# Performance work log

Measured on AMD Instinct MI355X. Metric: run time of the kernel, lower is better.

## Reference

```python
import jax, jax.numpy as jnp
import numpy as np

T, B, IN = 216, 16384, 8
H1, H2 = 16, 64


def _lstm_scan(xs, h0, c0, Wih, Whh, bih, bhh):
    # xs: [T, B, D_in]; returns all hidden states [T, B, H]
    def step(carry, x_t):
        h, c = carry
        g = x_t @ Wih.T + bih + h @ Whh.T + bhh  # [B, 4H]
        i, f, gg, o = jnp.split(g, 4, axis=-1)
        c = jax.nn.sigmoid(f) * c + jax.nn.sigmoid(i) * jnp.tanh(gg)
        h = jax.nn.sigmoid(o) * jnp.tanh(c)
        return (h, c), h
    (_, _), hs = jax.lax.scan(step, (h0, c0), xs)
    return hs


def setup_inputs() -> dict:
    key = jax.random.key(0)
    ks = jax.random.split(key, 24)
    def rn(k, shape, std):
        return jax.random.normal(k, shape, dtype=jnp.float32) * std
    # PyTorch LSTMCell/Linear default init: U(-1/sqrt(H), 1/sqrt(H)) -> use uniform
    def un(k, shape, bound):
        return jax.random.uniform(k, shape, dtype=jnp.float32, minval=-bound, maxval=bound)
    b1 = 1.0 / np.sqrt(H1)
    b2 = 1.0 / np.sqrt(H2)
    inp = {
        'x': jax.random.normal(ks[0], (T, B, IN), dtype=jnp.float32),
        # initial states: kaiming_normal_ with fan_in = last dim -> std = sqrt(2/fan_in)
        'h0f': rn(ks[1], (B, H1), np.sqrt(2.0 / H1)),
        'c0f': rn(ks[2], (B, H1), np.sqrt(2.0 / H1)),
        'h0b': rn(ks[3], (B, H1), np.sqrt(2.0 / H1)),
        'c0b': rn(ks[4], (B, H1), np.sqrt(2.0 / H1)),
        'h0m': rn(ks[5], (B, H2), np.sqrt(2.0 / H2)),
        'c0m': rn(ks[6], (B, H2), np.sqrt(2.0 / H2)),
        'Wih_f': un(ks[7], (4 * H1, IN), b1), 'Whh_f': un(ks[8], (4 * H1, H1), b1),
        'bih_f': un(ks[9], (4 * H1,), b1), 'bhh_f': un(ks[10], (4 * H1,), b1),
        'Wih_b': un(ks[11], (4 * H1, IN), b1), 'Whh_b': un(ks[12], (4 * H1, H1), b1),
        'bih_b': un(ks[13], (4 * H1,), b1), 'bhh_b': un(ks[14], (4 * H1,), b1),
        'Wih_m': un(ks[15], (4 * H2, 2 * H1), b2), 'Whh_m': un(ks[16], (4 * H2, H2), b2),
        'bih_m': un(ks[17], (4 * H2,), b2), 'bhh_m': un(ks[18], (4 * H2,), b2),
        'Wd': un(ks[19], (1, H2), b2), 'bd': un(ks[20], (1,), b2),
    }
    return inp


def reference(x, h0f, c0f, h0b, c0b, h0m, c0m,
              Wih_f, Whh_f, bih_f, bhh_f,
              Wih_b, Whh_b, bih_b, bhh_b,
              Wih_m, Whh_m, bih_m, bhh_m,
              Wd, bd):
    # forward direction LSTM over time
    hs_f = _lstm_scan(x, h0f, c0f, Wih_f, Whh_f, bih_f, bhh_f)          # [T,B,16]
    # backward direction: run on reversed sequence, then reverse outputs
    hs_b = _lstm_scan(x[::-1], h0b, c0b, Wih_b, Whh_b, bih_b, bhh_b)[::-1]  # [T,B,16]
    mid_in = jnp.concatenate([hs_f, hs_b], axis=-1)                     # [T,B,32]
    hs_m = _lstm_scan(mid_in, h0m, c0m, Wih_m, Whh_m, bih_m, bhh_m)     # [T,B,64]
    # dropout is identity in inference reference; dense 64->1 per step
    out = jnp.einsum('tbh,oh->tbo', hs_m, Wd) + bd                      # [T,B,1]
    return out[:, :, 0].T                                                # [B,T]
```

## Files before the change

kernel.cpp:

```cpp
#include <hip/hip_runtime.h>

#define TT 216
#define BB 16384
#define LOG2E 1.44269504088896340736f

typedef _Float16 h16;
typedef _Float16 half8 __attribute__((ext_vector_type(8)));
typedef float f32x4 __attribute__((ext_vector_type(4)));

__device__ __forceinline__ float rcp_f(float v) { return __builtin_amdgcn_rcpf(v); }
__device__ __forceinline__ float ex2(float v)   { return __builtin_amdgcn_exp2f(v); }

__device__ __forceinline__ float lstm_up(float pi, float pf, float pg, float po, float& cs)
{
    float ei = ex2(pi), ef = ex2(pf), eg = ex2(pg), eo = ex2(po);
    float Ei = 1.f + ei, Ef = 1.f + ef, Eg = 1.f + eg, Eo = 1.f + eo;
    float EiEg = Ei * Eg;
    float G = fmaf(2.f * LOG2E, Eg, -4.f * LOG2E);
    float N = fmaf(cs, EiEg, Ef * G);
    cs = N * rcp_f(Ef * EiEg);
    float pc = fminf(cs, 60.f);
    float Ec = 1.f + ex2(pc);
    return (Ec - 2.f) * rcp_f(Eo * Ec);
}

__global__ void prep_kernel(
    const float* __restrict__ Wih_f, const float* __restrict__ Whh_f,
    const float* __restrict__ bih_f, const float* __restrict__ bhh_f,
    const float* __restrict__ Wih_b, const float* __restrict__ Whh_b,
    const float* __restrict__ bih_b, const float* __restrict__ bhh_b,
    const float* __restrict__ Wih_m, const float* __restrict__ Whh_m,
    const float* __restrict__ bih_m, const float* __restrict__ bhh_m,
    h16* __restrict__ W1f, h16* __restrict__ W1b, h16* __restrict__ W2)
{
    int gtid = blockIdx.x * blockDim.x + threadIdx.x;
    int gs = gridDim.x * blockDim.x;
    for (int idx = gtid; idx < 64 * 32; idx += gs) {
        int n = idx >> 5, k = idx & 31;
        float a = ((n >> 4) == 2) ? 2.f * LOG2E : -LOG2E;
        float vf = 0.f, vb = 0.f;
        if (k < 8)        { vf = Wih_f[n * 8 + k];       vb = Wih_b[n * 8 + k]; }
        else if (k < 24)  { vf = Whh_f[n * 16 + k - 8];  vb = Whh_b[n * 16 + k - 8]; }
        else if (k == 24) { vf = bih_f[n] + bhh_f[n];    vb = bih_b[n] + bhh_b[n]; }
        W1f[idx] = (h16)(vf * a);
        W1b[idx] = (h16)(vb * a);
    }
    for (int idx = gtid; idx < 256 * 128; idx += gs) {
        int n = idx >> 7, k = idx & 127;
        float a = ((n >> 6) == 2) ? 2.f * LOG2E : -LOG2E;
        float v = 0.f;
        if (k < 32)       v = Wih_m[n * 32 + k];
        else if (k < 96)  v = Whh_m[n * 64 + k - 32];
        else if (k == 96) v = bih_m[n] + bhh_m[n];
        W2[idx] = (h16)(v * a);
    }
}

__global__ __launch_bounds__(256, 2) void small_lstm_kernel(
    const float* __restrict__ x,
    const float* __restrict__ h0f, const float* __restrict__ c0f,
    const float* __restrict__ h0b, const float* __restrict__ c0b,
    const h16* __restrict__ W1f, const h16* __restrict__ W1b,
    h16* __restrict__ hsf, h16* __restrict__ hsb)
{
    __shared__ __attribute__((aligned(16))) h16 hbuf[4][16][24];

    const int tid = threadIdx.x;
    const int wv = tid >> 6, lane = tid & 63;
    const int b = lane & 15, q = lane >> 4;

    const int wgid = blockIdx.x * 4 + wv;
    const int dir  = wgid & 1;
    const int base = (wgid >> 1) * 16;

    const float* h0 = dir ? h0b : h0f;
    const float* c0 = dir ? c0b : c0f;
    const h16* W1   = dir ? W1b : W1f;
    h16* hs = dir ? hsb : hsf;

    half8 bf0 = *(const half8*)(W1 + (0 * 16 + b) * 32 + q * 8);
    half8 bf1 = *(const half8*)(W1 + (1 * 16 + b) * 32 + q * 8);
    half8 bf2 = *(const half8*)(W1 + (2 * 16 + b) * 32 + q * 8);
    half8 bf3 = *(const half8*)(W1 + (3 * 16 + b) * 32 + q * 8);

    float cs0 = c0[(size_t)(base + q * 4 + 0) * 16 + b] * (2.f * LOG2E);
    float cs1 = c0[(size_t)(base + q * 4 + 1) * 16 + b] * (2.f * LOG2E);
    float cs2 = c0[(size_t)(base + q * 4 + 2) * 16 + b] * (2.f * LOG2E);
    float cs3 = c0[(size_t)(base + q * 4 + 3) * 16 + b] * (2.f * LOG2E);

    const int t0 = dir ? (TT - 1) : 0;
    const int t1 = dir ? (TT - 2) : 1;

    half8 af;
    if (q == 0) {
        const float* xp = x + ((size_t)t0 * BB + base + b) * 8;
        f32x4 u0 = *(const f32x4*)xp, u1 = *(const f32x4*)(xp + 4);
        af[0] = (h16)u0[0]; af[1] = (h16)u0[1]; af[2] = (h16)u0[2]; af[3] = (h16)u0[3];
        af[4] = (h16)u1[0]; af[5] = (h16)u1[1]; af[6] = (h16)u1[2]; af[7] = (h16)u1[3];
    } else if (q == 3) {
        af[0] = (h16)1.f;
        af[1] = (h16)0.f; af[2] = (h16)0.f; af[3] = (h16)0.f;
        af[4] = (h16)0.f; af[5] = (h16)0.f; af[6] = (h16)0.f; af[7] = (h16)0.f;
    } else {
        const float* hp = h0 + (size_t)(base + b) * 16 + (q - 1) * 8;
        f32x4 u0 = *(const f32x4*)hp, u1 = *(const f32x4*)(hp + 4);
        af[0] = (h16)u0[0]; af[1] = (h16)u0[1]; af[2] = (h16)u0[2]; af[3] = (h16)u0[3];
        af[4] = (h16)u1[0]; af[5] = (h16)u1[1]; af[6] = (h16)u1[2]; af[7] = (h16)u1[3];
    }

    f32x4 xf0 = {0.f, 0.f, 0.f, 0.f}, xf1 = {0.f, 0.f, 0.f, 0.f};
    if (q == 0) {
        const float* xp = x + ((size_t)t1 * BB + base + b) * 8;
        xf0 = *(const f32x4*)xp;
        xf1 = *(const f32x4*)(xp + 4);
    }

    for (int s = 0; s < TT; ++s) {
        const int t = dir ? (TT - 1 - s) : s;

        f32x4 z0 = {0.f, 0.f, 0.f, 0.f}, z1 = z0, z2 = z0, z3 = z0;
        z0 = __builtin_amdgcn_mfma_f32_16x16x32_f16(af, bf0, z0, 0, 0, 0);
        z1 = __builtin_amdgcn_mfma_f32_16x16x32_f16(af, bf1, z1, 0, 0, 0);
        z2 = __builtin_amdgcn_mfma_f32_16x16x32_f16(af, bf2, z2, 0, 0, 0);
        z3 = __builtin_amdgcn_mfma_f32_16x16x32_f16(af, bf3, z3, 0, 0, 0);

        half8 xh;
        xh[0] = (h16)xf0[0]; xh[1] = (h16)xf0[1]; xh[2] = (h16)xf0[2]; xh[3] = (h16)xf0[3];
        xh[4] = (h16)xf1[0]; xh[5] = (h16)xf1[1]; xh[6] = (h16)xf1[2]; xh[7] = (h16)xf1[3];
        {
            int sl = (s + 2 < TT) ? (s + 2) : (TT - 1);
            int tl = dir ? (TT - 1 - sl) : sl;
            if (q == 0) {
                const float* xp = x + ((size_t)tl * BB + base + b) * 8;
                xf0 = *(const f32x4*)xp;
                xf1 = *(const f32x4*)(xp + 4);
            }
        }

        float hh0 = lstm_up(z0[0], z1[0], z2[0], z3[0], cs0);
        float hh1 = lstm_up(z0[1], z1[1], z2[1], z3[1], cs1);
        float hh2 = lstm_up(z0[2], z1[2], z2[2], z3[2], cs2);
        float hh3 = lstm_up(z0[3], z1[3], z2[3], z3[3], cs3);

        hbuf[wv][q * 4 + 0][b] = (h16)hh0;
        hbuf[wv][q * 4 + 1][b] = (h16)hh1;
        hbuf[wv][q * 4 + 2][b] = (h16)hh2;
        hbuf[wv][q * 4 + 3][b] = (h16)hh3;
        asm volatile("s_waitcnt lgkmcnt(0)" ::: "memory");
        half8 hv = *(const half8*)&hbuf[wv][b][(q == 2) ? 8 : 0];

        if (q == 1 || q == 2)
            *(half8*)(hs + ((size_t)t * BB + base + b) * 16 + (q - 1) * 8) = hv;

        if (q == 0)      af = xh;
        else if (q != 3) af = hv;
    }
}

__global__ __launch_bounds__(256, 4) void mid_lstm_kernel(
    const h16* __restrict__ hsf, const h16* __restrict__ hsb,
    const float* __restrict__ h0m, const float* __restrict__ c0m,
    const h16* __restrict__ W2,
    const float* __restrict__ Wd, const float* __restrict__ bdp,
    float* __restrict__ out)
{
    __shared__ __attribute__((aligned(16))) h16 Xs[2][16][104];
    __shared__ float outbuf[16][55];

    const int tid = threadIdx.x;
    const int base = blockIdx.x * 16;
    const int wv = tid >> 6, lane = tid & 63, col = lane & 15, q = lane >> 4;

    half8 bfr[4][3];
    float bp[4];
#pragma unroll
    for (int p = 0; p < 4; ++p) {
        int n = p * 64 + wv * 16 + col;
#pragma unroll
        for (int kt = 0; kt < 3; ++kt)
            bfr[p][kt] = *(const half8*)(W2 + (size_t)n * 128 + kt * 32 + q * 8);
        bp[p] = (float)W2[(size_t)n * 128 + 96];
    }
    half8 dfr[2];
#pragma unroll
    for (int kt = 0; kt < 2; ++kt)
#pragma unroll
        for (int j = 0; j < 8; ++j)
            dfr[kt][j] = (col == 0) ? (h16)Wd[kt * 32 + q * 8 + j] : (h16)0.f;
    const float bdv = bdp[0];

    float cs[4];
#pragma unroll
    for (int r = 0; r < 4; ++r)
        cs[r] = c0m[(size_t)(base + q * 4 + r) * 64 + wv * 16 + col] * (2.f * LOG2E);

    const h16* hsrc = (wv == 1) ? hsb : hsf;
    const int srow = lane >> 1, su8 = (lane & 1) * 8;
    if (wv < 2 && lane < 32) {
        uint4 v = *(const uint4*)(hsrc + ((size_t)0 * BB + base + srow) * 16 + su8);
        *(uint4*)&Xs[0][srow][wv * 16 + su8] = v;
    }
    {
        int row = tid >> 4, u4 = (tid & 15) * 4;
        float4 v = *(const float4*)(h0m + (size_t)(base + row) * 64 + u4);
        h16* d = &Xs[0][row][32 + u4];
        d[0] = (h16)v.x; d[1] = (h16)v.y; d[2] = (h16)v.z; d[3] = (h16)v.w;
    }
    uint4 ra, rb;
    if (wv < 2 && lane < 32) {
        ra = *(const uint4*)(hsrc + ((size_t)1 * BB + base + srow) * 16 + su8);
        rb = *(const uint4*)(hsrc + ((size_t)2 * BB + base + srow) * 16 + su8);
    }
    __syncthreads();

    for (int t = 0; t < TT; ++t) {
        const int cur = t & 1, nxt = cur ^ 1;
        if (wv < 2 && lane < 32) {
            if (t < TT - 1)
                *(uint4*)&Xs[nxt][srow][wv * 16 + su8] = ra;
            ra = rb;
            int tl = (t + 3 < TT) ? (t + 3) : (TT - 1);
            rb = *(const uint4*)(hsrc + ((size_t)tl * BB + base + srow) * 16 + su8);
        }
        half8 af[3];
#pragma unroll
        for (int kt = 0; kt < 3; ++kt)
            af[kt] = *(const half8*)&Xs[cur][col][kt * 32 + q * 8];
        if (wv == 3 && t > 0) {
            f32x4 z = {0.f, 0.f, 0.f, 0.f};
            z = __builtin_amdgcn_mfma_f32_16x16x32_f16(af[1], dfr[0], z, 0, 0, 0);
            z = __builtin_amdgcn_mfma_f32_16x16x32_f16(af[2], dfr[1], z, 0, 0, 0);
            if (col == 0) {
                int tc = (t - 1) % 54;
#pragma unroll
                for (int r = 0; r < 4; ++r)
                    outbuf[q * 4 + r][tc] = z[r] + bdv;
            }
        }
        f32x4 acc[4];
#pragma unroll
        for (int p = 0; p < 4; ++p) {
            f32x4 z = {bp[p], bp[p], bp[p], bp[p]};
            z = __builtin_amdgcn_mfma_f32_16x16x32_f16(af[0], bfr[p][0], z, 0, 0, 0);
            z = __builtin_amdgcn_mfma_f32_16x16x32_f16(af[1], bfr[p][1], z, 0, 0, 0);
            z = __builtin_amdgcn_mfma_f32_16x16x32_f16(af[2], bfr[p][2], z, 0, 0, 0);
            acc[p] = z;
        }
#pragma unroll
        for (int r = 0; r < 4; ++r) {
            float h = lstm_up(acc[0][r], acc[1][r], acc[2][r], acc[3][r], cs[r]);
            Xs[nxt][q * 4 + r][32 + wv * 16 + col] = (h16)h;
        }
        if (t > 0 && (t % 54) == 0) {
            __syncthreads();
            int off = t - 54;
            for (int idx = tid; idx < 16 * 54; idx += 256) {
                int row = idx / 54, cc = idx - row * 54;
                out[(size_t)(base + row) * TT + off + cc] = outbuf[row][cc];
            }
        }
        __syncthreads();
    }
    if (wv == 3) {
        half8 a1 = *(const half8*)&Xs[0][col][32 + q * 8];
        half8 a2 = *(const half8*)&Xs[0][col][64 + q * 8];
        f32x4 z = {0.f, 0.f, 0.f, 0.f};
        z = __builtin_amdgcn_mfma_f32_16x16x32_f16(a1, dfr[0], z, 0, 0, 0);
        z = __builtin_amdgcn_mfma_f32_16x16x32_f16(a2, dfr[1], z, 0, 0, 0);
        if (col == 0)
#pragma unroll
            for (int r = 0; r < 4; ++r)
                outbuf[q * 4 + r][53] = z[r] + bdv;
    }
    __syncthreads();
    for (int idx = tid; idx < 16 * 54; idx += 256) {
        int row = idx / 54, cc = idx - row * 54;
        out[(size_t)(base + row) * TT + 162 + cc] = outbuf[row][cc];
    }
}

extern "C" void kernel_launch(void* const* d_in, const int* in_sizes, int n_in,
                              void* d_out, int out_size, void* d_ws, size_t ws_size,
                              hipStream_t stream)
{
    const float* x     = (const float*)d_in[0];
    const float* h0f   = (const float*)d_in[1];
    const float* c0f   = (const float*)d_in[2];
    const float* h0b   = (const float*)d_in[3];
    const float* c0b   = (const float*)d_in[4];
    const float* h0m   = (const float*)d_in[5];
    const float* c0m   = (const float*)d_in[6];
    const float* Wih_f = (const float*)d_in[7];
    const float* Whh_f = (const float*)d_in[8];
    const float* bih_f = (const float*)d_in[9];
    const float* bhh_f = (const float*)d_in[10];
    const float* Wih_b = (const float*)d_in[11];
    const float* Whh_b = (const float*)d_in[12];
    const float* bih_b = (const float*)d_in[13];
    const float* bhh_b = (const float*)d_in[14];
    const float* Wih_m = (const float*)d_in[15];
    const float* Whh_m = (const float*)d_in[16];
    const float* bih_m = (const float*)d_in[17];
    const float* bhh_m = (const float*)d_in[18];
    const float* Wd    = (const float*)d_in[19];
    const float* bd    = (const float*)d_in[20];

    char* ws = (char*)d_ws;
    h16* W1f = (h16*)(ws + 0);
    h16* W1b = (h16*)(ws + 4096);
    h16* W2  = (h16*)(ws + 8192);
    h16* hsf = (h16*)(ws + 73728);
    h16* hsb = (h16*)(ws + 73728 + (size_t)TT * BB * 16 * 2);

    prep_kernel<<<64, 256, 0, stream>>>(Wih_f, Whh_f, bih_f, bhh_f,
                                        Wih_b, Whh_b, bih_b, bhh_b,
                                        Wih_m, Whh_m, bih_m, bhh_m,
                                        W1f, W1b, W2);
    small_lstm_kernel<<<512, 256, 0, stream>>>(x, h0f, c0f, h0b, c0b,
                                               W1f, W1b, hsf, hsb);
    mid_lstm_kernel<<<1024, 256, 0, stream>>>(hsf, hsb, h0m, c0m, W2,
                                              Wd, bd, (float*)d_out);
}
```

Before: 669.9 us.

## Unroll bidirectional LSTM steps by four with deeper x prefetch and batched stores

The first-layer kernel now processes four timesteps per outer iteration. It keeps a four-slot register ring of prefetched x inputs, so loads are issued four steps ahead instead of two. Hidden-state stores to global memory are grouped at the end of each four-step block. The mid-LSTM kernel also raises wave priority around its MFMA block. The aim is to hide global load and store latency on the serial recurrence, at the cost of more registers and a TT divisible by 4.

```diff
diff --git a/kernel.cpp b/kernel.cpp
--- a/kernel.cpp
+++ b/kernel.cpp
@@ -89,7 +89,6 @@
     float cs3 = c0[(size_t)(base + q * 4 + 3) * 16 + b] * (2.f * LOG2E);
 
     const int t0 = dir ? (TT - 1) : 0;
-    const int t1 = dir ? (TT - 2) : 1;
 
     half8 af;
     if (q == 0) {
@@ -108,52 +107,67 @@
         af[4] = (h16)u1[0]; af[5] = (h16)u1[1]; af[6] = (h16)u1[2]; af[7] = (h16)u1[3];
     }
 
-    f32x4 xf0 = {0.f, 0.f, 0.f, 0.f}, xf1 = {0.f, 0.f, 0.f, 0.f};
+    f32x4 xr[4][2];
     if (q == 0) {
-        const float* xp = x + ((size_t)t1 * BB + base + b) * 8;
-        xf0 = *(const f32x4*)xp;
-        xf1 = *(const f32x4*)(xp + 4);
-    }
-
-    for (int s = 0; s < TT; ++s) {
-        const int t = dir ? (TT - 1 - s) : s;
-
-        f32x4 z0 = {0.f, 0.f, 0.f, 0.f}, z1 = z0, z2 = z0, z3 = z0;
-        z0 = __builtin_amdgcn_mfma_f32_16x16x32_f16(af, bf0, z0, 0, 0, 0);
-        z1 = __builtin_amdgcn_mfma_f32_16x16x32_f16(af, bf1, z1, 0, 0, 0);
-        z2 = __builtin_amdgcn_mfma_f32_16x16x32_f16(af, bf2, z2, 0, 0, 0);
-        z3 = __builtin_amdgcn_mfma_f32_16x16x32_f16(af, bf3, z3, 0, 0, 0);
-
-        half8 xh;
-        xh[0] = (h16)xf0[0]; xh[1] = (h16)xf0[1]; xh[2] = (h16)xf0[2]; xh[3] = (h16)xf0[3];
-        xh[4] = (h16)xf1[0]; xh[5] = (h16)xf1[1]; xh[6] = (h16)xf1[2]; xh[7] = (h16)xf1[3];
-        {
-            int sl = (s + 2 < TT) ? (s + 2) : (TT - 1);
-            int tl = dir ? (TT - 1 - sl) : sl;
+#pragma unroll
+        for (int u = 1; u <= 3; ++u) {
+            int tl = dir ? (TT - 1 - u) : u;
+            const float* xp = x + ((size_t)tl * BB + base + b) * 8;
+            xr[u][0] = *(const f32x4*)xp;
+            xr[u][1] = *(const f32x4*)(xp + 4);
+        }
+    }
+
+    for (int it = 0; it < TT / 4; ++it) {
+        half8 hst[4];
+#pragma unroll
+        for (int j = 0; j < 4; ++j) {
+            const int s = it * 4 + j;
+
+            f32x4 z0 = {0.f, 0.f, 0.f, 0.f}, z1 = z0, z2 = z0, z3 = z0;
+            z0 = __builtin_amdgcn_mfma_f32_16x16x32_f16(af, bf0, z0, 0, 0, 0);
+            z1 = __builtin_amdgcn_mfma_f32_16x16x32_f16(af, bf1, z1, 0, 0, 0);
+            z2 = __builtin_amdgcn_mfma_f32_16x16x32_f16(af, bf2, z2, 0, 0, 0);
+            z3 = __builtin_amdgcn_mfma_f32_16x16x32_f16(af, bf3, z3, 0, 0, 0);
+
+            half8 xh;
+            {
+                const f32x4 u0 = xr[(j + 1) & 3][0], u1 = xr[(j + 1) & 3][1];
+                xh[0] = (h16)u0[0]; xh[1] = (h16)u0[1]; xh[2] = (h16)u0[2]; xh[3] = (h16)u0[3];
+                xh[4] = (h16)u1[0]; xh[5] = (h16)u1[1]; xh[6] = (h16)u1[2]; xh[7] = (h16)u1[3];
+            }
             if (q == 0) {
+                int ut = (s + 4 < TT) ? (s + 4) : (TT - 1);
+                int tl = dir ? (TT - 1 - ut) : ut;
                 const float* xp = x + ((size_t)tl * BB + base + b) * 8;
-                xf0 = *(const f32x4*)xp;
-                xf1 = *(const f32x4*)(xp + 4);
-            }
-        }
-
-        float hh0 = lstm_up(z0[0], z1[0], z2[0], z3[0], cs0);
-        float hh1 = lstm_up(z0[1], z1[1], z2[1], z3[1], cs1);
-        float hh2 = lstm_up(z0[2], z1[2], z2[2], z3[2], cs2);
-        float hh3 = lstm_up(z0[3], z1[3], z2[3], z3[3], cs3);
-
-        hbuf[wv][q * 4 + 0][b] = (h16)hh0;
-        hbuf[wv][q * 4 + 1][b] = (h16)hh1;
-        hbuf[wv][q * 4 + 2][b] = (h16)hh2;
-        hbuf[wv][q * 4 + 3][b] = (h16)hh3;
-        asm volatile("s_waitcnt lgkmcnt(0)" ::: "memory");
-        half8 hv = *(const half8*)&hbuf[wv][b][(q == 2) ? 8 : 0];
-
-        if (q == 1 || q == 2)
-            *(half8*)(hs + ((size_t)t * BB + base + b) * 16 + (q - 1) * 8) = hv;
-
-        if (q == 0)      af = xh;
-        else if (q != 3) af = hv;
+                xr[j][0] = *(const f32x4*)xp;
+                xr[j][1] = *(const f32x4*)(xp + 4);
+            }
+
+            float hh0 = lstm_up(z0[0], z1[0], z2[0], z3[0], cs0);
+            float hh1 = lstm_up(z0[1], z1[1], z2[1], z3[1], cs1);
+            float hh2 = lstm_up(z0[2], z1[2], z2[2], z3[2], cs2);
+            float hh3 = lstm_up(z0[3], z1[3], z2[3], z3[3], cs3);
+
+            hbuf[wv][q * 4 + 0][b] = (h16)hh0;
+            hbuf[wv][q * 4 + 1][b] = (h16)hh1;
+            hbuf[wv][q * 4 + 2][b] = (h16)hh2;
+            hbuf[wv][q * 4 + 3][b] = (h16)hh3;
+            asm volatile("s_waitcnt lgkmcnt(0)" ::: "memory");
+            half8 hv = *(const half8*)&hbuf[wv][b][(q == 2) ? 8 : 0];
+            hst[j] = hv;
+
+            if (q == 0)      af = xh;
+            else if (q != 3) af = hv;
+        }
+        if (q == 1 || q == 2) {
+#pragma unroll
+            for (int j = 0; j < 4; ++j) {
+                int s = it * 4 + j;
+                int t = dir ? (TT - 1 - s) : s;
+                *(half8*)(hs + ((size_t)t * BB + base + b) * 16 + (q - 1) * 8) = hst[j];
+            }
+        }
     }
 }
 
@@ -238,6 +252,7 @@
             }
         }
         f32x4 acc[4];
+        __builtin_amdgcn_s_setprio(1);
 #pragma unroll
         for (int p = 0; p < 4; ++p) {
             f32x4 z = {bp[p], bp[p], bp[p], bp[p]};
@@ -246,6 +261,7 @@
             z = __builtin_amdgcn_mfma_f32_16x16x32_f16(af[2], bfr[p][2], z, 0, 0, 0);
             acc[p] = z;
         }
+        __builtin_amdgcn_s_setprio(0);
 #pragma unroll
         for (int r = 0; r < 4; ++r) {
             float h = lstm_up(acc[0][r], acc[1][r], acc[2][r], acc[3][r], cs[r]);
```

New measurement: 648.5 us. -3.2%, faster.
